# Kernel optimization log

Hardware: AMD Instinct MI355X
Metric: run time of the kernel (lower is better)

## Reference

```python
import jax, jax.numpy as jnp
import numpy as np
from itertools import combinations

# Static conv hyperparameters (match init_kwargs)
KH = KW = 3
SH = SW = 1
PH = PW = 1
DH = DW = 1
MAJ_DIM = 3  # = kernel_size[0]


def _maj_sim(x):
    """Vectorized bipolar majority-gate simulation. x: [B, n] -> [B].
    result = sum over majority subsets of prod((1+x)_in, (1-x)_out) / 2^(n-1) - 1
    """
    n = x.shape[1]
    thresh = (n + 1) // 2
    one_plus = 1.0 + x
    one_minus = 1.0 - x
    res = jnp.zeros(x.shape[0], dtype=x.dtype)
    for k in range(thresh, n + 1):
        for combo in combinations(range(n), k):
            mask = np.zeros(n, dtype=bool)
            mask[list(combo)] = True
            res = res + jnp.prod(jnp.where(jnp.asarray(mask), one_plus, one_minus), axis=1)
    return res / (2.0 ** (n - 1)) - 1.0


def _stack_maj_sim(x, maj_dim):
    """Stacked majority tree reduction along dim 1. x: [B, n] -> [B, n_final]."""
    B = x.shape[0]
    while x.shape[1] >= maj_dim:
        num_chunks = x.shape[1] // maj_dim
        if num_chunks == 0:
            break
        z = x[:, : num_chunks * maj_dim].reshape(B * num_chunks, maj_dim)
        x = _maj_sim(z).reshape(B, num_chunks)
    return x


def _unfold(x):
    """torch.nn.functional.unfold equivalent. x:[N,C,H,W] -> [N, C*KH*KW, L].
    Feature ordering matches torch: c-major, then kernel row, then kernel col."""
    N, C, H, W = x.shape
    H_out = (H + 2 * PH - DH * (KH - 1) - 1) // SH + 1
    W_out = (W + 2 * PW - DW * (KW - 1) - 1) // SW + 1
    xp = jnp.pad(x, ((0, 0), (0, 0), (PH, PH), (PW, PW)))
    slabs = [
        xp[:, :, i * DH : i * DH + SH * (H_out - 1) + 1 : SH,
              j * DW : j * DW + SW * (W_out - 1) + 1 : SW]
        for i in range(KH) for j in range(KW)
    ]
    p = jnp.stack(slabs, axis=2)  # [N, C, KH*KW, H_out, W_out]
    return p.reshape(N, C * KH * KW, H_out * W_out)


def setup_inputs() -> dict:
    key = jax.random.key(0)
    k1, k2 = jax.random.split(key)
    x = jax.random.normal(k1, (2, 27, 64, 64), dtype=jnp.float32)
    # kaiming-uniform-ish scale for fan_in = 27*3*3 = 243
    weight = jax.random.normal(k2, (32, 27, 3, 3), dtype=jnp.float32) * 0.06
    return {"x": x, "weight": weight}


def reference(x, weight):
    N, C, H, W = x.shape
    OC = weight.shape[0]
    H_out = (H + 2 * PH - DH * (KH - 1) - 1) // SH + 1
    W_out = (W + 2 * PW - DW * (KW - 1) - 1) // SW + 1
    patches = _unfold(x)                       # [N, F, L], F = C*KH*KW
    weight_flat = weight.reshape(OC, -1)       # [OC, F]
    # prod: [N, OC, F, L]
    prod = patches[:, None, :, :] * weight_flat[None, :, :, None]
    F_ = prod.shape[2]
    L = prod.shape[3]
    # reduce the feature dim via stacked majority simulation
    z = prod.transpose(0, 1, 3, 2).reshape(N * OC * L, F_)
    out = _stack_maj_sim(z, MAJ_DIM)           # [N*OC*L, 1]
    return out.reshape(N, OC, H_out, W_out)
```

## Files before the change

### kernel.cpp

```cpp
#include <hip/hip_runtime.h>

#define CIN 27
#define HH 64
#define WW 64
#define OC 32
#define TW 16
#define TH 16
#define RS 19
#define CS (18 * RS)
#define WS 12

__device__ __forceinline__ float maj3(float a, float b, float c) {
    float s = a + b + c;
    float p = a * b;
    return 0.5f * fmaf(-p, c, s);
}

__device__ __forceinline__ float2 pk_maj3(float2 a, float2 b, float2 c) {
    float2 r;
    r.x = maj3(a.x, b.x, c.x);
    r.y = maj3(a.y, b.y, c.y);
    return r;
}

__global__ __launch_bounds__(128) void sconv_maj_kernel(
    const float* __restrict__ x,
    const float* __restrict__ wgt,
    float* __restrict__ out)
{
    __shared__ __align__(16) float sw[CIN * WS];
    __shared__ float sx[CIN * CS];

    const int tx = threadIdx.x;
    const int ty = threadIdx.y;
    const int tid = ty * 8 + tx;
    const int tile_w0 = blockIdx.x * TW;
    const int tile_h0 = blockIdx.y * TH;
    const int n  = blockIdx.z >> 5;
    const int oc = blockIdx.z & 31;

    for (int i = tid; i < CIN * 9; i += 128) {
        int c = i / 9;
        int k = i - 9 * c;
        sw[c * WS + k] = wgt[oc * (CIN * 9) + i];
    }

    const float* xn = x + (size_t)n * (CIN * HH * WW);
    for (int pos = tid; pos < 18 * 18; pos += 128) {
        int r   = pos / 18;
        int col = pos - 18 * r;
        int gr = tile_h0 + r - 1;
        int gc = tile_w0 + col - 1;
        bool ok = (gr >= 0 && gr < HH && gc >= 0 && gc < WW);
        const float* gp = xn + gr * WW + gc;
        float* lp = sx + r * RS + col;
        #pragma unroll
        for (int c = 0; c < CIN; ++c) {
            lp[c * CS] = ok ? gp[c * (HH * WW)] : 0.0f;
        }
    }
    __syncthreads();

    float2 m2[CIN];
    #pragma unroll
    for (int c = 0; c < CIN; ++c) {
        float4 wa = *(const float4*)&sw[c * WS];
        float4 wb = *(const float4*)&sw[c * WS + 4];
        float  w8 = sw[c * WS + 8];
        const float wk[9] = {wa.x, wa.y, wa.z, wa.w, wb.x, wb.y, wb.z, wb.w, w8};

        float2 m1[3];
        #pragma unroll
        for (int ki = 0; ki < 3; ++ki) {
            const float* row = &sx[c * CS + (ty + ki) * RS + 2 * tx];
            float v0 = row[0], v1 = row[1], v2 = row[2], v3 = row[3];
            float w0 = wk[ki * 3 + 0], w1 = wk[ki * 3 + 1], w2 = wk[ki * 3 + 2];
            float2 p0 = make_float2(v0 * w0, v1 * w0);
            float2 p1 = make_float2(v1 * w1, v2 * w1);
            float2 p2 = make_float2(v2 * w2, v3 * w2);
            m1[ki] = pk_maj3(p0, p1, p2);
        }
        m2[c] = pk_maj3(m1[0], m1[1], m1[2]);
    }
    float2 m3[9];
    #pragma unroll
    for (int g = 0; g < 9; ++g)
        m3[g] = pk_maj3(m2[3 * g], m2[3 * g + 1], m2[3 * g + 2]);
    float2 m4a = pk_maj3(m3[0], m3[1], m3[2]);
    float2 m4b = pk_maj3(m3[3], m3[4], m3[5]);
    float2 m4c = pk_maj3(m3[6], m3[7], m3[8]);
    float2 res = pk_maj3(m4a, m4b, m4c);

    const int h = tile_h0 + ty;
    const int w = tile_w0 + 2 * tx;
    float2* po = (float2*)(out + (((size_t)n * OC + oc) * HH + h) * WW + w);
    *po = res;
}

extern "C" void kernel_launch(void* const* d_in, const int* in_sizes, int n_in,
                              void* d_out, int out_size, void* d_ws, size_t ws_size,
                              hipStream_t stream) {
    const float* x   = (const float*)d_in[0];
    const float* wgt = (const float*)d_in[1];
    float* out = (float*)d_out;

    dim3 block(8, 16, 1);
    dim3 grid(WW / TW, HH / TH, 2 * OC);
    sconv_maj_kernel<<<grid, block, 0, stream>>>(x, wgt, out);
}
```

Before: 77.84 us.

## Stage input channels in two halves to cut shared memory per block

```diff
diff --git a/kernel.cpp b/kernel.cpp
--- a/kernel.cpp
+++ b/kernel.cpp
@@ -1,19 +1,20 @@
 #include <hip/hip_runtime.h>
 
 #define CIN 27
+#define C0  14
+#define C1  13
 #define HH 64
 #define WW 64
 #define OC 32
 #define TW 16
 #define TH 16
-#define RS 19
+#define RS 24
 #define CS (18 * RS)
 #define WS 12
 
 __device__ __forceinline__ float maj3(float a, float b, float c) {
     float s = a + b + c;
-    float p = a * b;
-    return 0.5f * fmaf(-p, c, s);
+    return 0.5f * fmaf(-(a * b), c, s);
 }
 
 __device__ __forceinline__ float2 pk_maj3(float2 a, float2 b, float2 c) {
@@ -23,13 +24,66 @@
     return r;
 }
 
+struct SmemT {
+    float sw[CIN * WS];
+    __align__(16) float sx[C0 * CS];
+};
+
+template <int CBASE, int CNUM>
+__device__ __forceinline__ void stage_chunk(SmemT& sm, const float* __restrict__ xn,
+                                            int tid, int tile_h0, int tile_w0) {
+    #pragma unroll
+    for (int i = 0; i < 4; ++i) {
+        int slot = tid + 128 * i;
+        if (slot < CS) {
+            int r   = slot / RS;
+            int col = slot - r * RS;
+            int gr = tile_h0 + r - 1;
+            int gc = tile_w0 + col - 1;
+            bool ok = (col < 18) & ((unsigned)gr < (unsigned)HH) & ((unsigned)gc < (unsigned)WW);
+            int off = ok ? (gr * WW + gc) : 0;
+            #pragma unroll
+            for (int c = 0; c < CNUM; ++c) {
+                float raw = xn[(size_t)(CBASE + c) * (HH * WW) + off];
+                sm.sx[c * CS + slot] = ok ? raw : 0.0f;
+            }
+        }
+    }
+}
+
+template <int CBASE, int CNUM>
+__device__ __forceinline__ void compute_chunk(const SmemT& sm, float2* m2,
+                                              int tx, int ty) {
+    #pragma unroll
+    for (int c = 0; c < CNUM; ++c) {
+        const int cg = CBASE + c;
+        float4 wa = *(const float4*)&sm.sw[cg * WS];
+        float4 wb = *(const float4*)&sm.sw[cg * WS + 4];
+        float  w8 = sm.sw[cg * WS + 8];
+        const float wk[9] = {wa.x, wa.y, wa.z, wa.w, wb.x, wb.y, wb.z, wb.w, w8};
+
+        float2 m1[3];
+        #pragma unroll
+        for (int ki = 0; ki < 3; ++ki) {
+            const float2* prow = (const float2*)&sm.sx[c * CS + (ty + ki) * RS + 2 * tx];
+            float2 v01 = prow[0];
+            float2 v23 = prow[1];
+            float w0 = wk[ki * 3 + 0], w1 = wk[ki * 3 + 1], w2 = wk[ki * 3 + 2];
+            float2 p0 = make_float2(v01.x * w0, v01.y * w0);
+            float2 p1 = make_float2(v01.y * w1, v23.x * w1);
+            float2 p2 = make_float2(v23.x * w2, v23.y * w2);
+            m1[ki] = pk_maj3(p0, p1, p2);
+        }
+        m2[cg] = pk_maj3(m1[0], m1[1], m1[2]);
+    }
+}
+
 __global__ __launch_bounds__(128) void sconv_maj_kernel(
     const float* __restrict__ x,
     const float* __restrict__ wgt,
     float* __restrict__ out)
 {
-    __shared__ __align__(16) float sw[CIN * WS];
-    __shared__ float sx[CIN * CS];
+    __shared__ SmemT sm;
 
     const int tx = threadIdx.x;
     const int ty = threadIdx.y;
@@ -42,46 +96,21 @@
     for (int i = tid; i < CIN * 9; i += 128) {
         int c = i / 9;
         int k = i - 9 * c;
-        sw[c * WS + k] = wgt[oc * (CIN * 9) + i];
+        sm.sw[c * WS + k] = wgt[oc * (CIN * 9) + i];
     }
 
     const float* xn = x + (size_t)n * (CIN * HH * WW);
-    for (int pos = tid; pos < 18 * 18; pos += 128) {
-        int r   = pos / 18;
-        int col = pos - 18 * r;
-        int gr = tile_h0 + r - 1;
-        int gc = tile_w0 + col - 1;
-        bool ok = (gr >= 0 && gr < HH && gc >= 0 && gc < WW);
-        const float* gp = xn + gr * WW + gc;
-        float* lp = sx + r * RS + col;
-        #pragma unroll
-        for (int c = 0; c < CIN; ++c) {
-            lp[c * CS] = ok ? gp[c * (HH * WW)] : 0.0f;
-        }
-    }
+    float2 m2[CIN];
+
+    stage_chunk<0, C0>(sm, xn, tid, tile_h0, tile_w0);
+    __syncthreads();
+    compute_chunk<0, C0>(sm, m2, tx, ty);
     __syncthreads();
 
-    float2 m2[CIN];
-    #pragma unroll
-    for (int c = 0; c < CIN; ++c) {
-        float4 wa = *(const float4*)&sw[c * WS];
-        float4 wb = *(const float4*)&sw[c * WS + 4];
-        float  w8 = sw[c * WS + 8];
-        const float wk[9] = {wa.x, wa.y, wa.z, wa.w, wb.x, wb.y, wb.z, wb.w, w8};
+    stage_chunk<C0, C1>(sm, xn, tid, tile_h0, tile_w0);
+    __syncthreads();
+    compute_chunk<C0, C1>(sm, m2, tx, ty);
 
-        float2 m1[3];
-        #pragma unroll
-        for (int ki = 0; ki < 3; ++ki) {
-            const float* row = &sx[c * CS + (ty + ki) * RS + 2 * tx];
-            float v0 = row[0], v1 = row[1], v2 = row[2], v3 = row[3];
-            float w0 = wk[ki * 3 + 0], w1 = wk[ki * 3 + 1], w2 = wk[ki * 3 + 2];
-            float2 p0 = make_float2(v0 * w0, v1 * w0);
-            float2 p1 = make_float2(v1 * w1, v2 * w1);
-            float2 p2 = make_float2(v2 * w2, v3 * w2);
-            m1[ki] = pk_maj3(p0, p1, p2);
-        }
-        m2[c] = pk_maj3(m1[0], m1[1], m1[2]);
-    }
     float2 m3[9];
     #pragma unroll
     for (int g = 0; g < 9; ++g)
```

New measurement: 99.32 us. 1.28x slower.
